# Performance work log

Measured on AMD Instinct MI355X. Metric: run time of the kernel, lower is better.

## Reference

```python
import jax, jax.numpy as jnp
import numpy as np

N, E, IN_DIM, HID, L, H = 50000, 1600000, 32, 128, 3, 4
O = HID // H  # 32 per-head out_feats
PI = 3.141592653589793


def _glorot(key, shape):
    fan_in, fan_out = shape[-2], shape[-1]
    s = jnp.sqrt(6.0 / (fan_in + fan_out))
    return jax.random.uniform(key, shape, jnp.float32, -s, s)


def setup_inputs() -> dict:
    key = jax.random.key(0)
    ks = jax.random.split(key, 32)
    inp = {
        'node_feats': jax.random.normal(ks[0], (N, IN_DIM), jnp.float32),
        'src': jax.random.randint(ks[1], (E,), 0, N, jnp.int32),
        'dst': jax.random.randint(ks[2], (E,), 0, N, jnp.int32),
        # input projection
        'W_in': _glorot(ks[3], (IN_DIM, HID)), 'b_in': jnp.zeros((HID,), jnp.float32),
        # per-layer GATv2 params, stacked over L layers
        'W_src': _glorot(ks[4], (L, HID, HID)), 'b_src': jnp.zeros((L, HID), jnp.float32),
        'W_dst': _glorot(ks[5], (L, HID, HID)), 'b_dst': jnp.zeros((L, HID), jnp.float32),
        'attn': _glorot(ks[6], (L, H, O)),
        'ln_g': jnp.ones((L, HID), jnp.float32), 'ln_b': jnp.zeros((L, HID), jnp.float32),
        # node MLP + heads
        'W1': _glorot(ks[7], (HID, HID)), 'b1': jnp.zeros((HID,), jnp.float32),
        'W2': _glorot(ks[8], (HID, HID)), 'b2': jnp.zeros((HID,), jnp.float32),
        'Wa': _glorot(ks[9], (HID, 2)), 'ba': jnp.zeros((2,), jnp.float32),
        'Wg': _glorot(ks[10], (HID, 1)), 'bg': jnp.zeros((1,), jnp.float32),
        'Wal': _glorot(ks[11], (HID, 1)), 'bal': jnp.zeros((1,), jnp.float32),
        'Wn': _glorot(ks[12], (HID, 1)), 'bn': jnp.zeros((1,), jnp.float32),
        'Wt': _glorot(ks[13], (HID, 1)), 'bt': jnp.zeros((1,), jnp.float32),
    }
    return inp


def _segment_softmax(scores, seg, n):
    m = jax.ops.segment_max(scores, seg, num_segments=n)
    m = jnp.where(jnp.isfinite(m), m, 0.0)
    e = jnp.exp(scores - m[seg])
    s = jax.ops.segment_sum(e, seg, num_segments=n)
    return e / (s[seg] + 1e-9)


def _gatv2_layer(h, src, dst, Ws, bs, Wd, bd, a, g, b):
    n = h.shape[0]
    hs = (h @ Ws + bs).reshape(n, H, O)   # feat_src [N,H,O]
    hd = (h @ Wd + bd).reshape(n, H, O)   # feat_dst [N,H,O]
    e = jax.nn.leaky_relu(hs[src] + hd[dst], 0.2)     # [E,H,O]
    sc = jnp.einsum('eho,ho->eh', e, a)               # attention scores
    al = _segment_softmax(sc, dst, n)                 # softmax over in-edges
    rst = jax.ops.segment_sum(al[:, :, None] * hs[src], dst, num_segments=n)
    rst = rst + h.reshape(n, H, O)        # GATv2 residual (identity res_fc)
    h_new = rst.reshape(n, HID)
    x = h + h_new                         # encoder residual (dropout=eval)
    mu = jnp.mean(x, -1, keepdims=True)
    var = jnp.var(x, -1, keepdims=True)
    x = (x - mu) / jnp.sqrt(var + 1e-5) * g + b       # LayerNorm
    return jax.nn.relu(x)


def _forward(node_feats, src, dst, W_in, b_in, W_src, b_src, W_dst, b_dst, attn,
             ln_g, ln_b, W1, b1, W2, b2, Wa, ba, Wg, bg, Wal, bal, Wn, bn, Wt, bt):
    n = node_feats.shape[0]
    loops = jnp.arange(n, dtype=src.dtype)            # dgl.add_self_loop
    s = jnp.concatenate([src, loops])
    d = jnp.concatenate([dst, loops])
    h = node_feats @ W_in + b_in
    for l in range(L):
        h = _gatv2_layer(h, s, d, W_src[l], b_src[l], W_dst[l], b_dst[l],
                         attn[l], ln_g[l], ln_b[l])
    graph_emb = jnp.mean(h, axis=0, keepdims=True)    # dgl.mean_nodes, batch=1
    node_emb = h
    z = jax.nn.relu(jax.nn.relu(node_emb @ W1 + b1) @ W2 + b2)
    action_logits = z @ Wa + ba
    gamma = 5.0 * jax.nn.sigmoid((z @ Wg + bg)[:, 0])
    alpha = 2.0 * jax.nn.sigmoid((z @ Wal + bal)[:, 0])
    noise = 1.0 * jax.nn.sigmoid((z @ Wn + bn)[:, 0])
    theta = jnp.tanh((z @ Wt + bt)[:, 0]) * PI
    spawn_params = jnp.stack([gamma, alpha, noise, theta], axis=-1)
    return graph_emb, node_emb, action_logits, spawn_params


def reference(node_feats, src, dst, W_in, b_in, W_src, b_src, W_dst, b_dst, attn,
              ln_g, ln_b, W1, b1, W2, b2, Wa, ba, Wg, bg, Wal, bal, Wn, bn, Wt, bt):
    return _forward(node_feats, src, dst, W_in, b_in, W_src, b_src, W_dst, b_dst,
                    attn, ln_g, ln_b, W1, b1, W2, b2, Wa, ba, Wg, bg, Wal, bal,
                    Wn, bn, Wt, bt)
```

## Files before the change

kernel.cpp:

```cpp
#include <hip/hip_runtime.h>
#include <hip/hip_bf16.h>

#define HID 128
#define NHEAD 4
#define CAP 96

typedef __attribute__((ext_vector_type(8))) short bf16x8;
typedef __attribute__((ext_vector_type(4))) float f32x4;
typedef __attribute__((ext_vector_type(2))) float f32x2;

__device__ __forceinline__ unsigned pack2_bf16_rne(float lo, float hi) {
    unsigned a = __float_as_uint(lo);
    a = (a + 0x7fffu + ((a >> 16) & 1u)) >> 16;
    unsigned b = __float_as_uint(hi);
    b = (b + 0x7fffu + ((b >> 16) & 1u)) & 0xffff0000u;
    return a | b;
}

__device__ __forceinline__ unsigned short bf16_rne(float x) {
    unsigned u = __float_as_uint(x);
    u = (u + 0x7fffu + ((u >> 16) & 1u)) >> 16;
    return (unsigned short)u;
}

__device__ __forceinline__ f32x2 unpack_bf(unsigned u) {
    f32x2 r;
    r.x = __uint_as_float(u << 16);
    r.y = __uint_as_float(u & 0xffff0000u);
    return r;
}

__device__ __forceinline__ f32x2 leaky2(f32x2 q) {
    return __builtin_elementwise_max(q, q * 0.2f);
}

__device__ __forceinline__ float row_sum4(float x) {
    x += __int_as_float(__builtin_amdgcn_update_dpp(0, __float_as_int(x), 0xB1, 0xF, 0xF, true));
    x += __int_as_float(__builtin_amdgcn_update_dpp(0, __float_as_int(x), 0x4E, 0xF, 0xF, true));
    return x;
}

#define TILE2 1024
__global__ __launch_bounds__(256) void partition_and_prep(
    const int* __restrict__ src, const int* __restrict__ dst,
    int* __restrict__ tails, unsigned* __restrict__ buckets,
    int BCAP, int E, int qg, int ntiles,
    const float* __restrict__ W_src, const float* __restrict__ W_dst,
    const float* __restrict__ W1, const float* __restrict__ W2,
    unsigned short* __restrict__ Wt) {
    if ((int)blockIdx.x >= ntiles) {
        int mat = blockIdx.x - ntiles;
        const float* Wf = (mat < 3) ? (W_src + (size_t)mat * 16384)
                        : (mat < 6) ? (W_dst + (size_t)(mat - 3) * 16384)
                        : (mat == 6) ? W1 : W2;
        unsigned short* out = Wt + (size_t)mat * 16384;
        for (int idx = threadIdx.x; idx < 16384; idx += blockDim.x) {
            int k = idx >> 7, nn = idx & 127;
            out[nn * 128 + k] = bf16_rne(Wf[idx]);
        }
        return;
    }
    __shared__ int warr[4][8];
    __shared__ int base_sh[8];
    const int tid = threadIdx.x;
    const int wave = tid >> 6, lane = tid & 63;
    const int e0 = blockIdx.x * TILE2;
    const unsigned long long below = (1ULL << lane) - 1ULL;

    unsigned preg[4];
    int binr[4], rankr[4];
    int wcnt[8] = {0, 0, 0, 0, 0, 0, 0, 0};
#pragma unroll
    for (int j = 0; j < 4; ++j) {
        int idx = e0 + j * 256 + tid;
        bool ok = idx < E;
        int d = ok ? dst[idx] : 0;
        int s = ok ? src[idx] : 0;
        int g = ok ? (d / qg) : -1;
        int dl = d - g * qg;
        preg[j] = (unsigned)s | ((unsigned)dl << 16);
        binr[j] = g;
        int r = 0;
#pragma unroll
        for (int b = 0; b < 8; ++b) {
            unsigned long long mb = __ballot(g == b);
            if (g == b) r = wcnt[b] + (int)__popcll(mb & below);
            wcnt[b] += (int)__popcll(mb);
        }
        rankr[j] = r;
    }
    if (lane == 0) {
#pragma unroll
        for (int b = 0; b < 8; ++b) warr[wave][b] = wcnt[b];
    }
    __syncthreads();
    if (tid < 8) {
        int b = tid, tot = 0;
        int pre[4];
#pragma unroll
        for (int w = 0; w < 4; ++w) { pre[w] = tot; tot += warr[w][b]; }
        base_sh[b] = atomicAdd(&tails[b], tot);
#pragma unroll
        for (int w = 0; w < 4; ++w) warr[w][b] = pre[w];
    }
    __syncthreads();
#pragma unroll
    for (int j = 0; j < 4; ++j) {
        int g = binr[j];
        if (g >= 0) {
            int pos = base_sh[g] + warr[wave][g] + rankr[j];
            if (pos < BCAP) buckets[(size_t)g * BCAP + pos] = preg[j];
        }
    }
}

__global__ __launch_bounds__(256) void fill_slots(
    const unsigned* __restrict__ buckets, const int* __restrict__ tails,
    int* __restrict__ cnt, int* __restrict__ slots, int BCAP, int qg) {
    int g = blockIdx.x & 7;
    int blk = blockIdx.x >> 3;
    int nblk = gridDim.x >> 3;
    int c = tails[g]; if (c > BCAP) c = BCAP;
    int dbase = g * qg;
    const unsigned* b = buckets + (size_t)g * BCAP;
    for (int i = blk * 256 + threadIdx.x; i < c; i += nblk * 256) {
        unsigned p = b[i];
        int d = dbase + (int)(p >> 16);
        int pos = atomicAdd(&cnt[d], 1);
        if (pos < CAP) slots[(size_t)d * CAP + pos] = (int)(p & 0xFFFFu);
    }
}

#define GR 64
__global__ __launch_bounds__(256) void gemm_in(const float* __restrict__ A,
                                               const float* __restrict__ W,
                                               const float* __restrict__ bias,
                                               unsigned short* __restrict__ C16, int n) {
    const int K = 32;
    __shared__ __align__(16) float a_sh[GR * K];
    const int tid = threadIdx.x;
    const int tx = tid & 31;
    const int ty = tid >> 5;
    const int r0 = blockIdx.x * GR;

    for (int i = tid * 4; i < GR * K; i += 1024) {
        int r = i / K, k = i % K;
        int gr = r0 + r;
        float4 v = make_float4(0.f, 0.f, 0.f, 0.f);
        if (gr < n) v = *(const float4*)&A[(size_t)gr * K + k];
        *(float4*)&a_sh[i] = v;
    }
    __syncthreads();

    float4 acc[8];
#pragma unroll
    for (int r = 0; r < 8; ++r) acc[r] = make_float4(0.f, 0.f, 0.f, 0.f);

    const float* ab = &a_sh[ty * 8 * K];
    const float* wb = &W[tx * 4];

    for (int k = 0; k < K; k += 4) {
        float4 w0 = *(const float4*)&wb[(size_t)(k + 0) * 128];
        float4 w1 = *(const float4*)&wb[(size_t)(k + 1) * 128];
        float4 w2 = *(const float4*)&wb[(size_t)(k + 2) * 128];
        float4 w3 = *(const float4*)&wb[(size_t)(k + 3) * 128];
#pragma unroll
        for (int r = 0; r < 8; ++r) {
            float4 a4 = *(const float4*)&ab[r * K + k];
            acc[r].x = fmaf(a4.x, w0.x, acc[r].x);
            acc[r].y = fmaf(a4.x, w0.y, acc[r].y);
            acc[r].z = fmaf(a4.x, w0.z, acc[r].z);
            acc[r].w = fmaf(a4.x, w0.w, acc[r].w);
            acc[r].x = fmaf(a4.y, w1.x, acc[r].x);
            acc[r].y = fmaf(a4.y, w1.y, acc[r].y);
            acc[r].z = fmaf(a4.y, w1.z, acc[r].z);
            acc[r].w = fmaf(a4.y, w1.w, acc[r].w);
            acc[r].x = fmaf(a4.z, w2.x, acc[r].x);
            acc[r].y = fmaf(a4.z, w2.y, acc[r].y);
            acc[r].z = fmaf(a4.z, w2.z, acc[r].z);
            acc[r].w = fmaf(a4.z, w2.w, acc[r].w);
            acc[r].x = fmaf(a4.w, w3.x, acc[r].x);
            acc[r].y = fmaf(a4.w, w3.y, acc[r].y);
            acc[r].z = fmaf(a4.w, w3.z, acc[r].z);
            acc[r].w = fmaf(a4.w, w3.w, acc[r].w);
        }
    }

    float4 b4 = *(const float4*)&bias[tx * 4];
#pragma unroll
    for (int r = 0; r < 8; ++r) {
        int gr = r0 + ty * 8 + r;
        if (gr < n) {
            uint2 st;
            st.x = pack2_bf16_rne(acc[r].x + b4.x, acc[r].y + b4.y);
            st.y = pack2_bf16_rne(acc[r].z + b4.z, acc[r].w + b4.w);
            *(uint2*)&C16[(size_t)gr * 128 + tx * 4] = st;
        }
    }
}

template <bool RELU, bool F32OUT, bool BF16OUT>
__global__ __launch_bounds__(256) void gemm_mfma(
    const unsigned short* __restrict__ A16,
    const unsigned short* __restrict__ Bt16,
    const float* __restrict__ bias,
    float* __restrict__ Cf, unsigned short* __restrict__ C16, int n) {
    const int wave = threadIdx.x >> 6;
    const int lane = threadIdx.x & 63;
    const int r = lane & 15, g = lane >> 4;
    const int m0 = blockIdx.x * 64 + wave * 16;
    int ra = m0 + r; if (ra > n - 1) ra = n - 1;
    const bf16x8* Arow = (const bf16x8*)(A16 + (size_t)ra * 128);
    bf16x8 a0 = Arow[g];
    bf16x8 a1 = Arow[4 + g];
    bf16x8 a2 = Arow[8 + g];
    bf16x8 a3 = Arow[12 + g];
    const int row = m0 + r;
    const bool rok = row < n;
#pragma unroll
    for (int ct = 0; ct < 8; ++ct) {
        const bf16x8* Brow = (const bf16x8*)(Bt16 + (size_t)(ct * 16 + r) * 128);
        f32x4 acc = {0.f, 0.f, 0.f, 0.f};
        acc = __builtin_amdgcn_mfma_f32_16x16x32_bf16(Brow[g], a0, acc, 0, 0, 0);
        acc = __builtin_amdgcn_mfma_f32_16x16x32_bf16(Brow[4 + g], a1, acc, 0, 0, 0);
        acc = __builtin_amdgcn_mfma_f32_16x16x32_bf16(Brow[8 + g], a2, acc, 0, 0, 0);
        acc = __builtin_amdgcn_mfma_f32_16x16x32_bf16(Brow[12 + g], a3, acc, 0, 0, 0);
        const int col = ct * 16 + g * 4;
        float4 b4 = *(const float4*)&bias[col];
        float o0 = acc[0] + b4.x, o1 = acc[1] + b4.y;
        float o2 = acc[2] + b4.z, o3 = acc[3] + b4.w;
        if (RELU) {
            o0 = fmaxf(o0, 0.f); o1 = fmaxf(o1, 0.f);
            o2 = fmaxf(o2, 0.f); o3 = fmaxf(o3, 0.f);
        }
        if (rok) {
            if (F32OUT)
                *(float4*)&Cf[(size_t)row * 128 + col] = make_float4(o0, o1, o2, o3);
            if (BF16OUT) {
                uint2 st;
                st.x = pack2_bf16_rne(o0, o1);
                st.y = pack2_bf16_rne(o2, o3);
                *(uint2*)&C16[(size_t)row * 128 + col] = st;
            }
        }
    }
}

__global__ __launch_bounds__(256) void gemm_mfma_dual(
    const unsigned short* __restrict__ A16,
    const unsigned short* __restrict__ B1t, const unsigned short* __restrict__ B2t,
    const float* __restrict__ bias1, const float* __restrict__ bias2,
    unsigned short* __restrict__ C1, unsigned short* __restrict__ C2, int n) {
    const int wave = threadIdx.x >> 6;
    const int lane = threadIdx.x & 63;
    const int r = lane & 15, g = lane >> 4;
    const int m0 = blockIdx.x * 64 + wave * 16;
    int ra = m0 + r; if (ra > n - 1) ra = n - 1;
    const bf16x8* Arow = (const bf16x8*)(A16 + (size_t)ra * 128);
    bf16x8 a0 = Arow[g];
    bf16x8 a1 = Arow[4 + g];
    bf16x8 a2 = Arow[8 + g];
    bf16x8 a3 = Arow[12 + g];
    const int row = m0 + r;
    const bool rok = row < n;
#pragma unroll
    for (int ct = 0; ct < 8; ++ct) {
        const int col = ct * 16 + g * 4;
        {
            const bf16x8* Brow = (const bf16x8*)(B1t + (size_t)(ct * 16 + r) * 128);
            f32x4 acc = {0.f, 0.f, 0.f, 0.f};
            acc = __builtin_amdgcn_mfma_f32_16x16x32_bf16(Brow[g], a0, acc, 0, 0, 0);
            acc = __builtin_amdgcn_mfma_f32_16x16x32_bf16(Brow[4 + g], a1, acc, 0, 0, 0);
            acc = __builtin_amdgcn_mfma_f32_16x16x32_bf16(Brow[8 + g], a2, acc, 0, 0, 0);
            acc = __builtin_amdgcn_mfma_f32_16x16x32_bf16(Brow[12 + g], a3, acc, 0, 0, 0);
            float4 b4 = *(const float4*)&bias1[col];
            if (rok) {
                uint2 st;
                st.x = pack2_bf16_rne(acc[0] + b4.x, acc[1] + b4.y);
                st.y = pack2_bf16_rne(acc[2] + b4.z, acc[3] + b4.w);
                *(uint2*)&C1[(size_t)row * 128 + col] = st;
            }
        }
        {
            const bf16x8* Brow = (const bf16x8*)(B2t + (size_t)(ct * 16 + r) * 128);
            f32x4 acc = {0.f, 0.f, 0.f, 0.f};
            acc = __builtin_amdgcn_mfma_f32_16x16x32_bf16(Brow[g], a0, acc, 0, 0, 0);
            acc = __builtin_amdgcn_mfma_f32_16x16x32_bf16(Brow[4 + g], a1, acc, 0, 0, 0);
            acc = __builtin_amdgcn_mfma_f32_16x16x32_bf16(Brow[8 + g], a2, acc, 0, 0, 0);
            acc = __builtin_amdgcn_mfma_f32_16x16x32_bf16(Brow[12 + g], a3, acc, 0, 0, 0);
            float4 b4 = *(const float4*)&bias2[col];
            if (rok) {
                uint2 st;
                st.x = pack2_bf16_rne(acc[0] + b4.x, acc[1] + b4.y);
                st.y = pack2_bf16_rne(acc[2] + b4.z, acc[3] + b4.w);
                *(uint2*)&C2[(size_t)row * 128 + col] = st;
            }
        }
    }
}

template <bool LAST>
__global__ __launch_bounds__(256) void gat_aggregate(
    unsigned short* __restrict__ h16,
    const unsigned short* __restrict__ hs16,
    const unsigned short* __restrict__ hd16,
    const int* __restrict__ cnt,
    const int* __restrict__ slots,
    const float* __restrict__ attn,
    const float* __restrict__ ln_g, const float* __restrict__ ln_b,
    float* __restrict__ out_f32, int n) {
    int v = (blockIdx.x * blockDim.x + threadIdx.x) >> 6;
    int lane = threadIdx.x & 63;
    if (v >= n) return;
    const int lh = lane & 15;
    const int quarter = lane >> 4;
    const int f0 = lh * 8;
    const unsigned fb = (unsigned)lh << 4;

    const float L2E = 1.4426950408889634f;
    f32x2 av0, av1, av2, av3;
    {
        float4 aa = *(const float4*)&attn[f0];
        float4 ab = *(const float4*)&attn[f0 + 4];
        av0 = (f32x2){aa.x, aa.y} * L2E; av1 = (f32x2){aa.z, aa.w} * L2E;
        av2 = (f32x2){ab.x, ab.y} * L2E; av3 = (f32x2){ab.z, ab.w} * L2E;
    }
    const char* hsb = (const char*)hs16;
    f32x2 hd0, hd1, hd2, hd3;
    {
        uint4 wd = *(const uint4*)((const char*)hd16 + ((size_t)(unsigned)v << 8) + fb);
        hd0 = unpack_bf(wd.x); hd1 = unpack_bf(wd.y);
        hd2 = unpack_bf(wd.z); hd3 = unpack_bf(wd.w);
    }
    uint4 wv = *(const uint4*)(hsb + ((size_t)(unsigned)v << 8) + fb);
    f32x2 sv0 = unpack_bf(wv.x), sv1 = unpack_bf(wv.y);
    f32x2 sv2 = unpack_bf(wv.z), sv3 = unpack_bf(wv.w);
    float m;
    {
        f32x2 q0 = leaky2(sv0 + hd0), q1 = leaky2(sv1 + hd1);
        f32x2 q2 = leaky2(sv2 + hd2), q3 = leaky2(sv3 + hd3);
        f32x2 dt = q0 * av0; dt += q1 * av1; dt += q2 * av2; dt += q3 * av3;
        m = row_sum4(dt.x + dt.y);
    }
    const bool q0lane = (quarter == 0);
    float s = q0lane ? 1.f : 0.f;
    f32x2 acc0 = q0lane ? sv0 : (f32x2){0.f, 0.f};
    f32x2 acc1 = q0lane ? sv1 : (f32x2){0.f, 0.f};
    f32x2 acc2 = q0lane ? sv2 : (f32x2){0.f, 0.f};
    f32x2 acc3 = q0lane ? sv3 : (f32x2){0.f, 0.f};

    int deg = cnt[v]; if (deg > CAP) deg = CAP;
    const int* srow = slots + (size_t)v * CAP;
    int end4 = deg & ~3;

    auto process = [&](uint4 w) {
        f32x2 g0 = unpack_bf(w.x), g1 = unpack_bf(w.y);
        f32x2 g2 = unpack_bf(w.z), g3 = unpack_bf(w.w);
        f32x2 p0 = leaky2(g0 + hd0), p1 = leaky2(g1 + hd1);
        f32x2 p2 = leaky2(g2 + hd2), p3 = leaky2(g3 + hd3);
        f32x2 dt = p0 * av0; dt += p1 * av1; dt += p2 * av2; dt += p3 * av3;
        float sc = row_sum4(dt.x + dt.y);
        float d0 = sc - m;
        if (__builtin_expect(__any(d0 > 8.f), 0)) {
            float dmx = fmaxf(d0, __shfl_xor(d0, 16));
            dmx = fmaxf(dmx, __shfl_xor(dmx, 32));
            float mn = m + fmaxf(dmx, 0.f);
            float rr = exp2f(m - mn);
            s *= rr; acc0 *= rr; acc1 *= rr; acc2 *= rr; acc3 *= rr;
            m = mn; d0 = sc - m;
        }
        float e = exp2f(d0);
        s += e;
        acc0 += g0 * e; acc1 += g1 * e; acc2 += g2 * e; acc3 += g3 * e;
    };

    if (end4 > 0) {
        uint4 w = *(const uint4*)(hsb + ((size_t)(unsigned)srow[quarter] << 8) + fb);
        int un = (4 < end4) ? srow[4 + quarter] : 0;
        for (int i = 4; i < end4; i += 4) {
            uint4 wn = *(const uint4*)(hsb + ((size_t)(unsigned)un << 8) + fb);
            if (i + 4 < end4) un = srow[i + 4 + quarter];
            process(w);
            w = wn;
        }
        process(w);
    }
    if (end4 < deg) {
        int idx = end4 + quarter;
        bool act = idx < deg;
        int u = srow[act ? idx : end4];
        uint4 w = *(const uint4*)(hsb + ((size_t)(unsigned)u << 8) + fb);
        f32x2 g0 = unpack_bf(w.x), g1 = unpack_bf(w.y);
        f32x2 g2 = unpack_bf(w.z), g3 = unpack_bf(w.w);
        f32x2 p0 = leaky2(g0 + hd0), p1 = leaky2(g1 + hd1);
        f32x2 p2 = leaky2(g2 + hd2), p3 = leaky2(g3 + hd3);
        f32x2 dt = p0 * av0; dt += p1 * av1; dt += p2 * av2; dt += p3 * av3;
        float sc = row_sum4(dt.x + dt.y);
        float d0 = sc - m;
        float d0m = act ? d0 : -1e30f;
        if (__builtin_expect(__any(d0m > 8.f), 0)) {
            float dmx = fmaxf(d0m, __shfl_xor(d0m, 16));
            dmx = fmaxf(dmx, __shfl_xor(dmx, 32));
            float mn = m + fmaxf(dmx, 0.f);
            float rr = exp2f(m - mn);
            s *= rr; acc0 *= rr; acc1 *= rr; acc2 *= rr; acc3 *= rr;
            m = mn; d0 = sc - m;
        }
        float e = act ? exp2f(d0) : 0.f;
        s += e;
        acc0 += g0 * e; acc1 += g1 * e; acc2 += g2 * e; acc3 += g3 * e;
    }
#pragma unroll
    for (int d = 16; d <= 32; d <<= 1) {
        s += __shfl_xor(s, d);
        acc0.x += __shfl_xor(acc0.x, d); acc0.y += __shfl_xor(acc0.y, d);
        acc1.x += __shfl_xor(acc1.x, d); acc1.y += __shfl_xor(acc1.y, d);
        acc2.x += __shfl_xor(acc2.x, d); acc2.y += __shfl_xor(acc2.y, d);
        acc3.x += __shfl_xor(acc3.x, d); acc3.y += __shfl_xor(acc3.y, d);
    }
    float inv = 1.0f / (s + 1e-9f);

    f32x2 hv0, hv1, hv2, hv3;
    {
        uint4 wh = *(const uint4*)((const char*)h16 + ((size_t)(unsigned)v << 8) + fb);
        hv0 = unpack_bf(wh.x); hv1 = unpack_bf(wh.y);
        hv2 = unpack_bf(wh.z); hv3 = unpack_bf(wh.w);
    }
    f32x2 x0 = acc0 * inv + hv0 * 2.f;
    f32x2 x1 = acc1 * inv + hv1 * 2.f;
    f32x2 x2 = acc2 * inv + hv2 * 2.f;
    f32x2 x3 = acc3 * inv + hv3 * 2.f;

    f32x2 sum2 = (x0 + x1) + (x2 + x3);
    f32x2 sq2 = x0 * x0 + x1 * x1 + x2 * x2 + x3 * x3;
    float sum = sum2.x + sum2.y, sq = sq2.x + sq2.y;
#pragma unroll
    for (int d = 1; d < 64; d <<= 1) { sum += __shfl_xor(sum, d); sq += __shfl_xor(sq, d); }
    float mu = sum * (1.f / 512.f);
    float var = sq * (1.f / 512.f) - mu * mu;
    float rstd = rsqrtf(var + 1e-5f);
    f32x2 g0v, g1v, g2v, g3v, b0v, b1v, b2v, b3v;
    {
        float4 ga = *(const float4*)&ln_g[f0];
        float4 gb = *(const float4*)&ln_g[f0 + 4];
        float4 ba = *(const float4*)&ln_b[f0];
        float4 bb = *(const float4*)&ln_b[f0 + 4];
        g0v = (f32x2){ga.x, ga.y}; g1v = (f32x2){ga.z, ga.w};
        g2v = (f32x2){gb.x, gb.y}; g3v = (f32x2){gb.z, gb.w};
        b0v = (f32x2){ba.x, ba.y}; b1v = (f32x2){ba.z, ba.w};
        b2v = (f32x2){bb.x, bb.y}; b3v = (f32x2){bb.z, bb.w};
    }
    f32x2 zero = {0.f, 0.f};
    f32x2 y0 = __builtin_elementwise_max((x0 - mu) * rstd * g0v + b0v, zero);
    f32x2 y1 = __builtin_elementwise_max((x1 - mu) * rstd * g1v + b1v, zero);
    f32x2 y2 = __builtin_elementwise_max((x2 - mu) * rstd * g2v + b2v, zero);
    f32x2 y3 = __builtin_elementwise_max((x3 - mu) * rstd * g3v + b3v, zero);
    if (quarter == 0) {
        uint4 st;
        st.x = pack2_bf16_rne(y0.x, y0.y);
        st.y = pack2_bf16_rne(y1.x, y1.y);
        st.z = pack2_bf16_rne(y2.x, y2.y);
        st.w = pack2_bf16_rne(y3.x, y3.y);
        *(uint4*)((char*)h16 + ((size_t)v << 8) + fb) = st;
        if (LAST) {
            float* orow = &out_f32[(size_t)v * 128 + f0];
            *(float4*)orow = make_float4(y0.x, y0.y, y1.x, y1.y);
            *(float4*)(orow + 4) = make_float4(y2.x, y2.y, y3.x, y3.y);
        }
    }
}

__global__ __launch_bounds__(256) void mean_and_heads(
    const float* __restrict__ nemb, float* __restrict__ gacc,
    const float* __restrict__ z,
    const float* __restrict__ Wa, const float* __restrict__ ba,
    const float* __restrict__ Wg, const float* __restrict__ bg,
    const float* __restrict__ Wal, const float* __restrict__ bal,
    const float* __restrict__ Wn, const float* __restrict__ bn,
    const float* __restrict__ Wt, const float* __restrict__ bt,
    float* __restrict__ logits, float* __restrict__ spawn, int n, int MB) {
    if ((int)blockIdx.x < MB) {
        const float4* src = (const float4*)nemb;
        size_t n4 = (size_t)n * 32;
        int tid = threadIdx.x;
        size_t i = blockIdx.x * (size_t)256 + tid;
        size_t stride = (size_t)MB * 256;
        float ax = 0.f, ay = 0.f, az = 0.f, aw = 0.f;
        for (; i < n4; i += stride) {
            float4 v = src[i];
            ax += v.x; ay += v.y; az += v.z; aw += v.w;
        }
        __shared__ float4 sb[256];
        sb[tid] = make_float4(ax, ay, az, aw);
        __syncthreads();
        for (int off = 128; off >= 32; off >>= 1) {
            if (tid < off) {
                float4 o = sb[tid + off];
                sb[tid].x += o.x; sb[tid].y += o.y; sb[tid].z += o.z; sb[tid].w += o.w;
            }
            __syncthreads();
        }
        if (tid < 32) {
            float4 a = sb[tid];
            atomicAdd(&gacc[tid * 4 + 0], a.x);
            atomicAdd(&gacc[tid * 4 + 1], a.y);
            atomicAdd(&gacc[tid * 4 + 2], a.z);
            atomicAdd(&gacc[tid * 4 + 3], a.w);
        }
        return;
    }
    int v = (((int)blockIdx.x - MB) * blockDim.x + (int)threadIdx.x) >> 6;
    int lane = threadIdx.x & 63;
    if (v >= n) return;
    int f0 = lane * 2;
    float2 zv = *(const float2*)&z[(size_t)v * 128 + f0];
    float p0 = zv.x * Wa[f0 * 2]     + zv.y * Wa[(f0 + 1) * 2];
    float p1 = zv.x * Wa[f0 * 2 + 1] + zv.y * Wa[(f0 + 1) * 2 + 1];
    float p2 = zv.x * Wg[f0]  + zv.y * Wg[f0 + 1];
    float p3 = zv.x * Wal[f0] + zv.y * Wal[f0 + 1];
    float p4 = zv.x * Wn[f0]  + zv.y * Wn[f0 + 1];
    float p5 = zv.x * Wt[f0]  + zv.y * Wt[f0 + 1];
#pragma unroll
    for (int d = 1; d < 64; d <<= 1) {
        p0 += __shfl_xor(p0, d); p1 += __shfl_xor(p1, d); p2 += __shfl_xor(p2, d);
        p3 += __shfl_xor(p3, d); p4 += __shfl_xor(p4, d); p5 += __shfl_xor(p5, d);
    }
    if (lane == 0) {
        logits[(size_t)v * 2 + 0] = p0 + ba[0];
        logits[(size_t)v * 2 + 1] = p1 + ba[1];
        float gamma = 5.f / (1.f + __expf(-(p2 + bg[0])));
        float alpha = 2.f / (1.f + __expf(-(p3 + bal[0])));
        float noise = 1.f / (1.f + __expf(-(p4 + bn[0])));
        float theta = tanhf(p5 + bt[0]) * 3.14159265358979323846f;
        spawn[(size_t)v * 4 + 0] = gamma;
        spawn[(size_t)v * 4 + 1] = alpha;
        spawn[(size_t)v * 4 + 2] = noise;
        spawn[(size_t)v * 4 + 3] = theta;
    }
}

__global__ void graph_mean_final(const float* __restrict__ gacc, float* __restrict__ out, int n) {
    int c = threadIdx.x;
    out[c] = gacc[c] / (float)n;
}

extern "C" void kernel_launch(void* const* d_in, const int* in_sizes, int n_in,
                              void* d_out, int out_size, void* d_ws, size_t ws_size,
                              hipStream_t stream) {
    const float* node_feats = (const float*)d_in[0];
    const int*   src  = (const int*)d_in[1];
    const int*   dst  = (const int*)d_in[2];
    const float* W_in = (const float*)d_in[3];
    const float* b_in = (const float*)d_in[4];
    const float* W_src = (const float*)d_in[5];
    const float* b_src = (const float*)d_in[6];
    const float* W_dst = (const float*)d_in[7];
    const float* b_dst = (const float*)d_in[8];
    const float* attn  = (const float*)d_in[9];
    const float* ln_g  = (const float*)d_in[10];
    const float* ln_b  = (const float*)d_in[11];
    const float* W1 = (const float*)d_in[12]; const float* b1 = (const float*)d_in[13];
    const float* W2 = (const float*)d_in[14]; const float* b2 = (const float*)d_in[15];
    const float* Wa = (const float*)d_in[16]; const float* ba = (const float*)d_in[17];
    const float* Wg = (const float*)d_in[18]; const float* bg = (const float*)d_in[19];
    const float* Wal = (const float*)d_in[20]; const float* bal = (const float*)d_in[21];
    const float* Wn = (const float*)d_in[22]; const float* bn = (const float*)d_in[23];
    const float* Wt = (const float*)d_in[24]; const float* bt = (const float*)d_in[25];

    const int n = in_sizes[0] / 32;
    const int E = in_sizes[1];
    const int qg = (n + 7) / 8;
    const int BCAP = 240 * 1024;
    const int ntiles = (E + TILE2 - 1) / TILE2;

    char* ws = (char*)d_ws;
    size_t off = 0;
    auto alloc = [&](size_t bytes) -> void* {
        void* p = ws + off;
        off = (off + bytes + 255) & ~(size_t)255;
        return p;
    };
    float* Bz  = (float*)alloc((size_t)n * 128 * 4);
    unsigned short* h16  = (unsigned short*)alloc((size_t)n * 128 * 2);
    unsigned short* hs16 = (unsigned short*)alloc((size_t)n * 128 * 2);
    unsigned short* hd16 = (unsigned short*)alloc((size_t)n * 128 * 2);
    unsigned short* Wt16 = (unsigned short*)alloc((size_t)8 * 16384 * 2);
    int* cnt   = (int*)alloc((size_t)n * 4);
    int* slots = (int*)alloc((size_t)n * CAP * 4);
    unsigned* buckets = (unsigned*)alloc((size_t)8 * BCAP * 4);
    int* tails = (int*)alloc(8 * 4);
    float* gacc = (float*)alloc(128 * 4);

    float* out = (float*)d_out;
    float* out_gemb   = out;
    float* out_nemb   = out + 128;
    float* out_logits = out + 128 + (size_t)n * 128;
    float* out_spawn  = out_logits + (size_t)n * 2;

    hipMemsetAsync(cnt, 0, (size_t)n * 4, stream);
    hipMemsetAsync(tails, 0, 8 * 4, stream);
    hipMemsetAsync(gacc, 0, 128 * 4, stream);

    partition_and_prep<<<ntiles + 8, 256, 0, stream>>>(
        src, dst, tails, buckets, BCAP, E, qg, ntiles, W_src, W_dst, W1, W2, Wt16);
    fill_slots<<<2048, 256, 0, stream>>>(buckets, tails, cnt, slots, BCAP, qg);

    int gemm_grid = (n + GR - 1) / GR;
    int mfma_grid = (n + 63) / 64;

    gemm_in<<<gemm_grid, 256, 0, stream>>>(node_feats, W_in, b_in, h16, n);

    for (int l = 0; l < 3; ++l) {
        gemm_mfma_dual<<<mfma_grid, 256, 0, stream>>>(
            h16, Wt16 + (size_t)l * 16384, Wt16 + (size_t)(3 + l) * 16384,
            b_src + l * 128, b_dst + l * 128, hs16, hd16, n);
        if (l == 2)
            gat_aggregate<true><<<(n + 3) / 4, 256, 0, stream>>>(
                h16, hs16, hd16, cnt, slots, attn + l * 128, ln_g + l * 128,
                ln_b + l * 128, out_nemb, n);
        else
            gat_aggregate<false><<<(n + 3) / 4, 256, 0, stream>>>(
                h16, hs16, hd16, cnt, slots, attn + l * 128, ln_g + l * 128,
                ln_b + l * 128, nullptr, n);
    }

    gemm_mfma<true, false, true><<<mfma_grid, 256, 0, stream>>>(
        h16, Wt16 + (size_t)6 * 16384, b1, nullptr, hs16, n);
    gemm_mfma<true, true, false><<<mfma_grid, 256, 0, stream>>>(
        hs16, Wt16 + (size_t)7 * 16384, b2, Bz, nullptr, n);

    const int MB = 512;
    mean_and_heads<<<MB + (n + 3) / 4, 256, 0, stream>>>(
        out_nemb, gacc, Bz, Wa, ba, Wg, bg, Wal, bal, Wn, bn, Wt, bt,
        out_logits, out_spawn, n, MB);
    graph_mean_final<<<1, 128, 0, stream>>>(gacc, out_gemb, n);
}
```

Before: 555.5 us.

## Fuse MLP GEMMs, output heads and graph mean into one kernel

Replaces the two MLP MFMA GEMM launches and the separate heads/mean kernel with a single kernel. Each 64-row block computes relu(h@W1+b1) into LDS as bf16, feeds it to the second GEMM, stages the fp32 z tile in LDS, and evaluates the six head projections from there. The extra blocks that compute the graph-mean reduction are appended to the same grid. This removes the global round trips for the intermediate z1 (bf16) and z (fp32) and two kernel launches. In exchange it uses about 33 KB of LDS per block and serialises a 16-row head loop per wave.

```diff
diff --git a/kernel.cpp b/kernel.cpp
--- a/kernel.cpp
+++ b/kernel.cpp
@@ -195,53 +195,6 @@
             st.x = pack2_bf16_rne(acc[r].x + b4.x, acc[r].y + b4.y);
             st.y = pack2_bf16_rne(acc[r].z + b4.z, acc[r].w + b4.w);
             *(uint2*)&C16[(size_t)gr * 128 + tx * 4] = st;
-        }
-    }
-}
-
-template <bool RELU, bool F32OUT, bool BF16OUT>
-__global__ __launch_bounds__(256) void gemm_mfma(
-    const unsigned short* __restrict__ A16,
-    const unsigned short* __restrict__ Bt16,
-    const float* __restrict__ bias,
-    float* __restrict__ Cf, unsigned short* __restrict__ C16, int n) {
-    const int wave = threadIdx.x >> 6;
-    const int lane = threadIdx.x & 63;
-    const int r = lane & 15, g = lane >> 4;
-    const int m0 = blockIdx.x * 64 + wave * 16;
-    int ra = m0 + r; if (ra > n - 1) ra = n - 1;
-    const bf16x8* Arow = (const bf16x8*)(A16 + (size_t)ra * 128);
-    bf16x8 a0 = Arow[g];
-    bf16x8 a1 = Arow[4 + g];
-    bf16x8 a2 = Arow[8 + g];
-    bf16x8 a3 = Arow[12 + g];
-    const int row = m0 + r;
-    const bool rok = row < n;
-#pragma unroll
-    for (int ct = 0; ct < 8; ++ct) {
-        const bf16x8* Brow = (const bf16x8*)(Bt16 + (size_t)(ct * 16 + r) * 128);
-        f32x4 acc = {0.f, 0.f, 0.f, 0.f};
-        acc = __builtin_amdgcn_mfma_f32_16x16x32_bf16(Brow[g], a0, acc, 0, 0, 0);
-        acc = __builtin_amdgcn_mfma_f32_16x16x32_bf16(Brow[4 + g], a1, acc, 0, 0, 0);
-        acc = __builtin_amdgcn_mfma_f32_16x16x32_bf16(Brow[8 + g], a2, acc, 0, 0, 0);
-        acc = __builtin_amdgcn_mfma_f32_16x16x32_bf16(Brow[12 + g], a3, acc, 0, 0, 0);
-        const int col = ct * 16 + g * 4;
-        float4 b4 = *(const float4*)&bias[col];
-        float o0 = acc[0] + b4.x, o1 = acc[1] + b4.y;
-        float o2 = acc[2] + b4.z, o3 = acc[3] + b4.w;
-        if (RELU) {
-            o0 = fmaxf(o0, 0.f); o1 = fmaxf(o1, 0.f);
-            o2 = fmaxf(o2, 0.f); o3 = fmaxf(o3, 0.f);
-        }
-        if (rok) {
-            if (F32OUT)
-                *(float4*)&Cf[(size_t)row * 128 + col] = make_float4(o0, o1, o2, o3);
-            if (BF16OUT) {
-                uint2 st;
-                st.x = pack2_bf16_rne(o0, o1);
-                st.y = pack2_bf16_rne(o2, o3);
-                *(uint2*)&C16[(size_t)row * 128 + col] = st;
-            }
         }
     }
 }
@@ -470,32 +423,35 @@
     }
 }
 
-__global__ __launch_bounds__(256) void mean_and_heads(
-    const float* __restrict__ nemb, float* __restrict__ gacc,
-    const float* __restrict__ z,
+__global__ __launch_bounds__(256) void mlp_heads_mean(
+    const unsigned short* __restrict__ h16,
+    const unsigned short* __restrict__ W1t, const unsigned short* __restrict__ W2t,
+    const float* __restrict__ b1, const float* __restrict__ b2,
     const float* __restrict__ Wa, const float* __restrict__ ba,
     const float* __restrict__ Wg, const float* __restrict__ bg,
     const float* __restrict__ Wal, const float* __restrict__ bal,
     const float* __restrict__ Wn, const float* __restrict__ bn,
     const float* __restrict__ Wt, const float* __restrict__ bt,
-    float* __restrict__ logits, float* __restrict__ spawn, int n, int MB) {
-    if ((int)blockIdx.x < MB) {
-        const float4* src = (const float4*)nemb;
+    float* __restrict__ logits, float* __restrict__ spawn,
+    const float* __restrict__ nemb, float* __restrict__ gacc,
+    int n, int nMLP, int MB) {
+    if ((int)blockIdx.x >= nMLP) {
+        const float4* srcp = (const float4*)nemb;
         size_t n4 = (size_t)n * 32;
         int tid = threadIdx.x;
-        size_t i = blockIdx.x * (size_t)256 + tid;
+        size_t i = ((int)blockIdx.x - nMLP) * (size_t)256 + tid;
         size_t stride = (size_t)MB * 256;
         float ax = 0.f, ay = 0.f, az = 0.f, aw = 0.f;
         for (; i < n4; i += stride) {
-            float4 v = src[i];
+            float4 v = srcp[i];
             ax += v.x; ay += v.y; az += v.z; aw += v.w;
         }
         __shared__ float4 sb[256];
         sb[tid] = make_float4(ax, ay, az, aw);
         __syncthreads();
-        for (int off = 128; off >= 32; off >>= 1) {
-            if (tid < off) {
-                float4 o = sb[tid + off];
+        for (int off2 = 128; off2 >= 32; off2 >>= 1) {
+            if (tid < off2) {
+                float4 o = sb[tid + off2];
                 sb[tid].x += o.x; sb[tid].y += o.y; sb[tid].z += o.z; sb[tid].w += o.w;
             }
             __syncthreads();
@@ -509,33 +465,106 @@
         }
         return;
     }
-    int v = (((int)blockIdx.x - MB) * blockDim.x + (int)threadIdx.x) >> 6;
-    int lane = threadIdx.x & 63;
-    if (v >= n) return;
-    int f0 = lane * 2;
-    float2 zv = *(const float2*)&z[(size_t)v * 128 + f0];
-    float p0 = zv.x * Wa[f0 * 2]     + zv.y * Wa[(f0 + 1) * 2];
-    float p1 = zv.x * Wa[f0 * 2 + 1] + zv.y * Wa[(f0 + 1) * 2 + 1];
-    float p2 = zv.x * Wg[f0]  + zv.y * Wg[f0 + 1];
-    float p3 = zv.x * Wal[f0] + zv.y * Wal[f0 + 1];
-    float p4 = zv.x * Wn[f0]  + zv.y * Wn[f0 + 1];
-    float p5 = zv.x * Wt[f0]  + zv.y * Wt[f0 + 1];
-#pragma unroll
-    for (int d = 1; d < 64; d <<= 1) {
-        p0 += __shfl_xor(p0, d); p1 += __shfl_xor(p1, d); p2 += __shfl_xor(p2, d);
-        p3 += __shfl_xor(p3, d); p4 += __shfl_xor(p4, d); p5 += __shfl_xor(p5, d);
-    }
-    if (lane == 0) {
-        logits[(size_t)v * 2 + 0] = p0 + ba[0];
-        logits[(size_t)v * 2 + 1] = p1 + ba[1];
-        float gamma = 5.f / (1.f + __expf(-(p2 + bg[0])));
-        float alpha = 2.f / (1.f + __expf(-(p3 + bal[0])));
-        float noise = 1.f / (1.f + __expf(-(p4 + bn[0])));
-        float theta = tanhf(p5 + bt[0]) * 3.14159265358979323846f;
-        spawn[(size_t)v * 4 + 0] = gamma;
-        spawn[(size_t)v * 4 + 1] = alpha;
-        spawn[(size_t)v * 4 + 2] = noise;
-        spawn[(size_t)v * 4 + 3] = theta;
+    __shared__ __align__(16) char lds_raw[64 * 132 * 4];
+    unsigned short* z1l = (unsigned short*)lds_raw;
+    float* zl = (float*)lds_raw;
+
+    const int wave = threadIdx.x >> 6;
+    const int lane = threadIdx.x & 63;
+    const int r = lane & 15, g = lane >> 4;
+    const int m0 = blockIdx.x * 64 + wave * 16;
+    int ra = m0 + r; if (ra > n - 1) ra = n - 1;
+    const int lrow = wave * 16 + r;
+
+    {
+        const bf16x8* Arow = (const bf16x8*)(h16 + (size_t)ra * 128);
+        bf16x8 a0 = Arow[g];
+        bf16x8 a1 = Arow[4 + g];
+        bf16x8 a2 = Arow[8 + g];
+        bf16x8 a3 = Arow[12 + g];
+#pragma unroll
+        for (int ct = 0; ct < 8; ++ct) {
+            const bf16x8* Brow = (const bf16x8*)(W1t + (size_t)(ct * 16 + r) * 128);
+            f32x4 acc = {0.f, 0.f, 0.f, 0.f};
+            acc = __builtin_amdgcn_mfma_f32_16x16x32_bf16(Brow[g], a0, acc, 0, 0, 0);
+            acc = __builtin_amdgcn_mfma_f32_16x16x32_bf16(Brow[4 + g], a1, acc, 0, 0, 0);
+            acc = __builtin_amdgcn_mfma_f32_16x16x32_bf16(Brow[8 + g], a2, acc, 0, 0, 0);
+            acc = __builtin_amdgcn_mfma_f32_16x16x32_bf16(Brow[12 + g], a3, acc, 0, 0, 0);
+            const int col = ct * 16 + g * 4;
+            float4 bb = *(const float4*)&b1[col];
+            uint2 st;
+            st.x = pack2_bf16_rne(fmaxf(acc[0] + bb.x, 0.f), fmaxf(acc[1] + bb.y, 0.f));
+            st.y = pack2_bf16_rne(fmaxf(acc[2] + bb.z, 0.f), fmaxf(acc[3] + bb.w, 0.f));
+            *(uint2*)&z1l[lrow * 136 + col] = st;
+        }
+    }
+    __syncthreads();
+    f32x4 zc[8];
+    {
+        const unsigned short* zrow = &z1l[lrow * 136];
+        bf16x8 a0 = *(const bf16x8*)&zrow[g * 8];
+        bf16x8 a1 = *(const bf16x8*)&zrow[32 + g * 8];
+        bf16x8 a2 = *(const bf16x8*)&zrow[64 + g * 8];
+        bf16x8 a3 = *(const bf16x8*)&zrow[96 + g * 8];
+#pragma unroll
+        for (int ct = 0; ct < 8; ++ct) {
+            const bf16x8* Brow = (const bf16x8*)(W2t + (size_t)(ct * 16 + r) * 128);
+            f32x4 acc = {0.f, 0.f, 0.f, 0.f};
+            acc = __builtin_amdgcn_mfma_f32_16x16x32_bf16(Brow[g], a0, acc, 0, 0, 0);
+            acc = __builtin_amdgcn_mfma_f32_16x16x32_bf16(Brow[4 + g], a1, acc, 0, 0, 0);
+            acc = __builtin_amdgcn_mfma_f32_16x16x32_bf16(Brow[8 + g], a2, acc, 0, 0, 0);
+            acc = __builtin_amdgcn_mfma_f32_16x16x32_bf16(Brow[12 + g], a3, acc, 0, 0, 0);
+            const int col = ct * 16 + g * 4;
+            float4 bb = *(const float4*)&b2[col];
+            zc[ct][0] = fmaxf(acc[0] + bb.x, 0.f);
+            zc[ct][1] = fmaxf(acc[1] + bb.y, 0.f);
+            zc[ct][2] = fmaxf(acc[2] + bb.z, 0.f);
+            zc[ct][3] = fmaxf(acc[3] + bb.w, 0.f);
+        }
+    }
+    __syncthreads();
+#pragma unroll
+    for (int ct = 0; ct < 8; ++ct) {
+        const int col = ct * 16 + g * 4;
+        *(f32x4*)&zl[lrow * 132 + col] = zc[ct];
+    }
+    __syncthreads();
+    {
+        const int f0 = lane * 2;
+        float wa_a0 = Wa[f0 * 2], wa_a1 = Wa[f0 * 2 + 1];
+        float wa_b0 = Wa[(f0 + 1) * 2], wa_b1 = Wa[(f0 + 1) * 2 + 1];
+        float2 wgv = *(const float2*)&Wg[f0];
+        float2 walv = *(const float2*)&Wal[f0];
+        float2 wnv = *(const float2*)&Wn[f0];
+        float2 wtv = *(const float2*)&Wt[f0];
+        for (int t = 0; t < 16; ++t) {
+            int v = blockIdx.x * 64 + wave * 16 + t;
+            if (v >= n) break;
+            float2 zv = *(const float2*)&zl[(wave * 16 + t) * 132 + f0];
+            float p0 = zv.x * wa_a0 + zv.y * wa_b0;
+            float p1 = zv.x * wa_a1 + zv.y * wa_b1;
+            float p2 = zv.x * wgv.x + zv.y * wgv.y;
+            float p3 = zv.x * walv.x + zv.y * walv.y;
+            float p4 = zv.x * wnv.x + zv.y * wnv.y;
+            float p5 = zv.x * wtv.x + zv.y * wtv.y;
+#pragma unroll
+            for (int d = 1; d < 64; d <<= 1) {
+                p0 += __shfl_xor(p0, d); p1 += __shfl_xor(p1, d); p2 += __shfl_xor(p2, d);
+                p3 += __shfl_xor(p3, d); p4 += __shfl_xor(p4, d); p5 += __shfl_xor(p5, d);
+            }
+            if (lane == 0) {
+                logits[(size_t)v * 2 + 0] = p0 + ba[0];
+                logits[(size_t)v * 2 + 1] = p1 + ba[1];
+                float gamma = 5.f / (1.f + __expf(-(p2 + bg[0])));
+                float alpha = 2.f / (1.f + __expf(-(p3 + bal[0])));
+                float noise = 1.f / (1.f + __expf(-(p4 + bn[0])));
+                float theta = tanhf(p5 + bt[0]) * 3.14159265358979323846f;
+                spawn[(size_t)v * 4 + 0] = gamma;
+                spawn[(size_t)v * 4 + 1] = alpha;
+                spawn[(size_t)v * 4 + 2] = noise;
+                spawn[(size_t)v * 4 + 3] = theta;
+            }
+        }
     }
 }
 
@@ -580,7 +609,6 @@
         off = (off + bytes + 255) & ~(size_t)255;
         return p;
     };
-    float* Bz  = (float*)alloc((size_t)n * 128 * 4);
     unsigned short* h16  = (unsigned short*)alloc((size_t)n * 128 * 2);
     unsigned short* hs16 = (unsigned short*)alloc((size_t)n * 128 * 2);
     unsigned short* hd16 = (unsigned short*)alloc((size_t)n * 128 * 2);
@@ -624,14 +652,10 @@
                 ln_b + l * 128, nullptr, n);
     }
 
-    gemm_mfma<true, false, true><<<mfma_grid, 256, 0, stream>>>(
-        h16, Wt16 + (size_t)6 * 16384, b1, nullptr, hs16, n);
-    gemm_mfma<true, true, false><<<mfma_grid, 256, 0, stream>>>(
-        hs16, Wt16 + (size_t)7 * 16384, b2, Bz, nullptr, n);
-
     const int MB = 512;
-    mean_and_heads<<<MB + (n + 3) / 4, 256, 0, stream>>>(
-        out_nemb, gacc, Bz, Wa, ba, Wg, bg, Wal, bal, Wn, bn, Wt, bt,
-        out_logits, out_spawn, n, MB);
+    mlp_heads_mean<<<mfma_grid + MB, 256, 0, stream>>>(
+        h16, Wt16 + (size_t)6 * 16384, Wt16 + (size_t)7 * 16384, b1, b2,
+        Wa, ba, Wg, bg, Wal, bal, Wn, bn, Wt, bt,
+        out_logits, out_spawn, out_nemb, gacc, n, mfma_grid, MB);
     graph_mean_final<<<1, 128, 0, stream>>>(gacc, out_gemb, n);
 }
```

Result: faster. 534.6 us (-3.7%).
